# Optimization experiments

Measured on AMD Instinct MI355X. Metric: run time of the kernel, lower is better.

The kernel has to match this reference:

```python
import jax, jax.numpy as jnp
import numpy as np

FRAME = 160
NTAPS = 16
T = 2400
SCALE = 255.0 / 32768.0
SCALE_1 = 32768.0 / 255.0
LOG256 = float(np.log(256.0))

def u2l(u):
    u = u - 128.0
    s = jnp.sign(u)
    a = jnp.abs(u)
    return s * SCALE_1 * (jnp.exp(a / 128.0 * LOG256) - 1.0)

def l2u(x):
    s = jnp.sign(x)
    a = jnp.abs(x)
    u = s * (128.0 * jnp.log1p(SCALE * a) / LOG256)
    return jnp.clip(128.0 + u, 0.0, 255.0)

def setup_inputs() -> dict:
    key = jax.random.key(0)
    k1, k2 = jax.random.split(key)
    sig = jax.random.uniform(k1, (2048, T, 1), dtype=jnp.float32) * 255.0  # mu-law samples in [0,255]
    lpc = jax.random.normal(k2, (2048, 15, NTAPS), dtype=jnp.float32) * 0.1  # per-frame LPC coeffs
    return {"sig": sig, "lpc": lpc}

def reference(sig, lpc):
    xt = u2l(sig)  # [B,T,1] linear-domain signal
    # zero-pad 16 samples at front: zp[b, k] = xt[b, k-16]
    zp = jnp.concatenate([jnp.zeros_like(xt[:, :NTAPS, :]), xt], axis=1)[..., 0]  # [B,T+16]
    # tap i at time t reads zp[:, 16 - i + t]  (i.e. xt[t - i])
    idx = NTAPS + jnp.arange(T)[:, None] - jnp.arange(NTAPS)[None, :]  # [T,16]
    windows = zp[:, idx]  # [B,T,16]
    rep_lpc = jnp.repeat(lpc, FRAME, axis=1)  # [B,T,16]
    pred = -jnp.sum(rep_lpc * windows, axis=2, keepdims=True)  # [B,T,1]
    return l2u(pred)
```

## Files before the change

### kernel.cpp

```cpp
#include <hip/hip_runtime.h>
#include <hip/hip_bf16.h>
#include <math.h>

#define T_LEN   2400
#define NTAPS   16
#define FRAME   160
#define NFRAMES 15
#define NGROUPS (T_LEN / 4)
#define SCALE_C    (255.0f / 32768.0f)
#define SCALE_1_C  (32768.0f / 255.0f)

__device__ __forceinline__ float u2l_f(float uv) {
    float u = uv - 128.0f;
    float a = fabsf(u);
    float m = SCALE_1_C * (exp2f(a * 0.0625f) - 1.0f);
    return copysignf(m, u);
}

__device__ __forceinline__ float l2u_f(float x) {
    float a = fabsf(x);
    float u = 16.0f * log2f(fmaf(SCALE_C, a, 1.0f));
    u = copysignf(u, x);
    float r = 128.0f + u;
    return fminf(fmaxf(r, 0.0f), 255.0f);
}

__global__ __launch_bounds__(256) void diff_pred_kernel(
        const float* __restrict__ sig,
        const float* __restrict__ lpc,
        float* __restrict__ out) {
    __shared__ __align__(16) float xt_s[NTAPS + T_LEN];
    __shared__ __align__(16) float lpc_s[NFRAMES * NTAPS];

    const int b   = blockIdx.x;
    const int tid = threadIdx.x;

    const float* sig_b = sig + (size_t)b * T_LEN;
    const float* lpc_b = lpc + (size_t)b * (NFRAMES * NTAPS);

    if (tid < NTAPS) xt_s[tid] = 0.0f;
    if (tid < NFRAMES * NTAPS) lpc_s[tid] = lpc_b[tid];

    const float4* sig4 = (const float4*)sig_b;
    for (int i = tid; i < NGROUPS; i += 256) {
        float4 v = sig4[i];
        float4 d;
        d.x = u2l_f(v.x);
        d.y = u2l_f(v.y);
        d.z = u2l_f(v.z);
        d.w = u2l_f(v.w);
        *(float4*)&xt_s[NTAPS + 4 * i] = d;
    }
    __syncthreads();

    float4* out4 = (float4*)(out + (size_t)b * T_LEN);
    for (int i = tid; i < NGROUPS; i += 256) {
        const int t0 = 4 * i;
        const int f  = i / 40;

        const float4 c0 = *(const float4*)&lpc_s[f * NTAPS + 0];
        const float4 c1 = *(const float4*)&lpc_s[f * NTAPS + 4];
        const float4 c2 = *(const float4*)&lpc_s[f * NTAPS + 8];
        const float4 c3 = *(const float4*)&lpc_s[f * NTAPS + 12];
        float c[NTAPS] = {c0.x, c0.y, c0.z, c0.w, c1.x, c1.y, c1.z, c1.w,
                          c2.x, c2.y, c2.z, c2.w, c3.x, c3.y, c3.z, c3.w};

        const float4 w0 = *(const float4*)&xt_s[t0 + 0];
        const float4 w1 = *(const float4*)&xt_s[t0 + 4];
        const float4 w2 = *(const float4*)&xt_s[t0 + 8];
        const float4 w3 = *(const float4*)&xt_s[t0 + 12];
        const float4 w4 = *(const float4*)&xt_s[t0 + 16];
        float w[20] = {w0.x, w0.y, w0.z, w0.w, w1.x, w1.y, w1.z, w1.w,
                       w2.x, w2.y, w2.z, w2.w, w3.x, w3.y, w3.z, w3.w,
                       w4.x, w4.y, w4.z, w4.w};

        float acc[4] = {0.0f, 0.0f, 0.0f, 0.0f};
        #pragma unroll
        for (int j = 0; j < NTAPS; ++j) {
            #pragma unroll
            for (int k = 0; k < 4; ++k) {
                acc[k] = fmaf(c[j], w[16 + k - j], acc[k]);
            }
        }

        float4 o;
        o.x = l2u_f(-acc[0]);
        o.y = l2u_f(-acc[1]);
        o.z = l2u_f(-acc[2]);
        o.w = l2u_f(-acc[3]);
        out4[i] = o;
    }
}

extern "C" void kernel_launch(void* const* d_in, const int* in_sizes, int n_in,
                              void* d_out, int out_size, void* d_ws, size_t ws_size,
                              hipStream_t stream) {
    const float* sig = (const float*)d_in[0];
    const float* lpc = (const float*)d_in[1];
    float* out = (float*)d_out;

    const int batch = in_sizes[0] / T_LEN;
    diff_pred_kernel<<<batch, 256, 0, stream>>>(sig, lpc, out);
}
```

Before: 78.29 us.

## Drop shared-memory staging; each thread loads its own halo from global

Result: no change. 78.80 us (+0.7%).

```diff
diff --git a/kernel.cpp b/kernel.cpp
--- a/kernel.cpp
+++ b/kernel.cpp
@@ -1,12 +1,15 @@
 #include <hip/hip_runtime.h>
-#include <hip/hip_bf16.h>
 #include <math.h>
 
 #define T_LEN   2400
 #define NTAPS   16
 #define FRAME   160
 #define NFRAMES 15
-#define NGROUPS (T_LEN / 4)
+#define OPT     8
+#define GPR     (T_LEN / OPT)
+#define WLEN    (NTAPS + OPT)
+#define NLD     (WLEN / 4)
+
 #define SCALE_C    (255.0f / 32768.0f)
 #define SCALE_1_C  (32768.0f / 255.0f)
 
@@ -28,68 +31,63 @@
 __global__ __launch_bounds__(256) void diff_pred_kernel(
         const float* __restrict__ sig,
         const float* __restrict__ lpc,
-        float* __restrict__ out) {
-    __shared__ __align__(16) float xt_s[NTAPS + T_LEN];
-    __shared__ __align__(16) float lpc_s[NFRAMES * NTAPS];
+        float* __restrict__ out,
+        int total) {
+    const int g = blockIdx.x * 256 + threadIdx.x;
+    if (g >= total) return;
 
-    const int b   = blockIdx.x;
-    const int tid = threadIdx.x;
+    const int row = g / GPR;
+    const int rt  = g - row * GPR;
+    const int t0  = rt * OPT;
 
-    const float* sig_b = sig + (size_t)b * T_LEN;
-    const float* lpc_b = lpc + (size_t)b * (NFRAMES * NTAPS);
+    const float* sig_b = sig + (size_t)row * T_LEN;
 
-    if (tid < NTAPS) xt_s[tid] = 0.0f;
-    if (tid < NFRAMES * NTAPS) lpc_s[tid] = lpc_b[tid];
+    float4 rv[NLD];
+    #pragma unroll
+    for (int r = 0; r < NLD; ++r) {
+        const int off  = t0 - NTAPS + 4 * r;
+        const int soff = off < 0 ? 0 : off;
+        float4 v = *(const float4*)(sig_b + soff);
+        if (off < 0) v = make_float4(128.0f, 128.0f, 128.0f, 128.0f);
+        rv[r] = v;
+    }
 
-    const float4* sig4 = (const float4*)sig_b;
-    for (int i = tid; i < NGROUPS; i += 256) {
-        float4 v = sig4[i];
-        float4 d;
-        d.x = u2l_f(v.x);
-        d.y = u2l_f(v.y);
-        d.z = u2l_f(v.z);
-        d.w = u2l_f(v.w);
-        *(float4*)&xt_s[NTAPS + 4 * i] = d;
+    const int f = rt / (FRAME / OPT);
+    const float* lpc_b = lpc + (size_t)row * (NFRAMES * NTAPS) + f * NTAPS;
+    const float4 c0 = *(const float4*)(lpc_b + 0);
+    const float4 c1 = *(const float4*)(lpc_b + 4);
+    const float4 c2 = *(const float4*)(lpc_b + 8);
+    const float4 c3 = *(const float4*)(lpc_b + 12);
+    const float c[NTAPS] = {c0.x, c0.y, c0.z, c0.w, c1.x, c1.y, c1.z, c1.w,
+                            c2.x, c2.y, c2.z, c2.w, c3.x, c3.y, c3.z, c3.w};
+
+    float w[WLEN];
+    #pragma unroll
+    for (int r = 0; r < NLD; ++r) {
+        w[4*r+0] = u2l_f(rv[r].x);
+        w[4*r+1] = u2l_f(rv[r].y);
+        w[4*r+2] = u2l_f(rv[r].z);
+        w[4*r+3] = u2l_f(rv[r].w);
     }
-    __syncthreads();
 
-    float4* out4 = (float4*)(out + (size_t)b * T_LEN);
-    for (int i = tid; i < NGROUPS; i += 256) {
-        const int t0 = 4 * i;
-        const int f  = i / 40;
+    float acc[OPT] = {0.0f, 0.0f, 0.0f, 0.0f, 0.0f, 0.0f, 0.0f, 0.0f};
+    #pragma unroll
+    for (int j = 0; j < NTAPS; ++j) {
+        #pragma unroll
+        for (int k = 0; k < OPT; ++k) {
+            acc[k] = fmaf(c[j], w[NTAPS + k - j], acc[k]);
+        }
+    }
 
-        const float4 c0 = *(const float4*)&lpc_s[f * NTAPS + 0];
-        const float4 c1 = *(const float4*)&lpc_s[f * NTAPS + 4];
-        const float4 c2 = *(const float4*)&lpc_s[f * NTAPS + 8];
-        const float4 c3 = *(const float4*)&lpc_s[f * NTAPS + 12];
-        float c[NTAPS] = {c0.x, c0.y, c0.z, c0.w, c1.x, c1.y, c1.z, c1.w,
-                          c2.x, c2.y, c2.z, c2.w, c3.x, c3.y, c3.z, c3.w};
+    float4 o0, o1;
+    o0.x = l2u_f(-acc[0]); o0.y = l2u_f(-acc[1]);
+    o0.z = l2u_f(-acc[2]); o0.w = l2u_f(-acc[3]);
+    o1.x = l2u_f(-acc[4]); o1.y = l2u_f(-acc[5]);
+    o1.z = l2u_f(-acc[6]); o1.w = l2u_f(-acc[7]);
 
-        const float4 w0 = *(const float4*)&xt_s[t0 + 0];
-        const float4 w1 = *(const float4*)&xt_s[t0 + 4];
-        const float4 w2 = *(const float4*)&xt_s[t0 + 8];
-        const float4 w3 = *(const float4*)&xt_s[t0 + 12];
-        const float4 w4 = *(const float4*)&xt_s[t0 + 16];
-        float w[20] = {w0.x, w0.y, w0.z, w0.w, w1.x, w1.y, w1.z, w1.w,
-                       w2.x, w2.y, w2.z, w2.w, w3.x, w3.y, w3.z, w3.w,
-                       w4.x, w4.y, w4.z, w4.w};
-
-        float acc[4] = {0.0f, 0.0f, 0.0f, 0.0f};
-        #pragma unroll
-        for (int j = 0; j < NTAPS; ++j) {
-            #pragma unroll
-            for (int k = 0; k < 4; ++k) {
-                acc[k] = fmaf(c[j], w[16 + k - j], acc[k]);
-            }
-        }
-
-        float4 o;
-        o.x = l2u_f(-acc[0]);
-        o.y = l2u_f(-acc[1]);
-        o.z = l2u_f(-acc[2]);
-        o.w = l2u_f(-acc[3]);
-        out4[i] = o;
-    }
+    float* out_b = out + (size_t)row * T_LEN + t0;
+    *(float4*)(out_b + 0) = o0;
+    *(float4*)(out_b + 4) = o1;
 }
 
 extern "C" void kernel_launch(void* const* d_in, const int* in_sizes, int n_in,
@@ -100,5 +98,7 @@
     float* out = (float*)d_out;
 
     const int batch = in_sizes[0] / T_LEN;
-    diff_pred_kernel<<<batch, 256, 0, stream>>>(sig, lpc, out);
+    const int total = batch * GPR;
+    const int nblk  = (total + 255) / 256;
+    diff_pred_kernel<<<nblk, 256, 0, stream>>>(sig, lpc, out, total);
 }
```
